# Kernel tuning notes

Hardware: AMD Instinct MI355X
Metric: run time of the kernel (lower is better)

The kernel has to match this reference:

```python
import jax, jax.numpy as jnp
import numpy as np

B, T1, T2, D, H, NL, DFF, NC = 4, 128, 128, 512, 4, 4, 2048, 5
SQRT2 = 1.4142135623730951


def _ln(x, w, b, eps=1e-12):
    m = jnp.mean(x, -1, keepdims=True)
    v = jnp.mean((x - m) ** 2, -1, keepdims=True)
    return w * (x - m) / jnp.sqrt(v + eps) + b


def _gelu(x):  # erf-based gelu, as in source
    return x * 0.5 * (1.0 + jax.lax.erf(x / SQRT2))


def _mha(x, wq, bq, wk, bk, wv, bv, wo, bo):
    b, t, d = x.shape
    dk = d // H
    q = (x @ wq + bq).reshape(b, t, H, dk).transpose(0, 2, 1, 3)
    k = (x @ wk + bk).reshape(b, t, H, dk).transpose(0, 2, 1, 3)
    v = (x @ wv + bv).reshape(b, t, H, dk).transpose(0, 2, 1, 3)
    p = jax.nn.softmax(jnp.einsum('bhqd,bhkd->bhqk', q, k) / jnp.sqrt(jnp.float32(dk)), -1)
    o = jnp.einsum('bhqk,bhkd->bhqd', p, v).transpose(0, 2, 1, 3).reshape(b, t, d)
    return o @ wo + bo


def _encode(x, pos_emb, pe_w, pe_b, Wq, bq, Wk, bk, Wv, bv, Wo, bo,
            ff1_w, ff1_b, ff2_w, ff2_b, lnin_w, lnin_b, lnout_w, lnout_b):
    t = x.shape[1]
    x = _ln(x + pos_emb[:t], pe_w, pe_b)  # PositionalEncoding (dropout=0 eval)
    for i in range(Wq.shape[0]):  # EncoderLayer x NL
        x = x + _mha(x, Wq[i], bq[i], Wk[i], bk[i], Wv[i], bv[i], Wo[i], bo[i])
        h = _ln(x, lnin_w[i], lnin_b[i])
        x = x + (_gelu(h @ ff1_w[i] + ff1_b[i]) @ ff2_w[i] + ff2_b[i])
        x = _ln(x, lnout_w[i], lnout_b[i])
    return x


def _forward(q_emb, a_emb, qa_relation, aq_relation, concept_emb, pos_emb, pe_w, pe_b,
             Wq, bq, Wk, bk, Wv, bv, Wo, bo, ff1_w, ff1_b, ff2_w, ff2_b,
             lnin_w, lnin_b, lnout_w, lnout_b, sim_Wq, sim_bq, sim_Wk, sim_bk, cls_w, cls_b):
    enc = lambda x: _encode(x, pos_emb, pe_w, pe_b, Wq, bq, Wk, bk, Wv, bv, Wo, bo,
                            ff1_w, ff1_b, ff2_w, ff2_b, lnin_w, lnin_b, lnout_w, lnout_b)
    qe = enc(q_emb)   # [B,T1,D]
    ae = enc(a_emb)   # [B,T2,D]
    # ConceptEncoding: relation one-hots -> concept embedding mix
    hL = qa_relation @ concept_emb   # [B,T1,T2,D]
    hR = aq_relation @ concept_emb   # [B,T2,T1,D]
    # SimAttn: note source uses fwK for BOTH key and value, so v == k exactly
    q = qe @ sim_Wq + sim_bq
    k = ae @ sim_Wk + sim_bk
    kR = jnp.transpose(k[:, :, None, :] + hR, (0, 2, 1, 3))  # [B,T1,T2,D]
    scores = jnp.sum((q[:, :, None, :] + hL) * kR, axis=-1)   # [B,T1,T2]
    p = jax.nn.softmax(scores, -1)
    # sharpening branch (default sharpening=True): re-softmax the attention probs
    p = jnp.clip(jax.nn.softmax(1000.0 * p, -1), 0.0, 1.0)
    # value path: v + hR transposed == kR since v == k
    x = jnp.einsum('bts,btsd->btd', p, kR)                    # [B,T1,D]
    return jnp.mean(x, 1) @ cls_w + cls_b                     # [B,3]


def setup_inputs() -> dict:
    key = jax.random.key(0)
    rk = lambda i: jax.random.fold_in(key, i)
    w = lambda i, shape: 0.02 * jax.random.normal(rk(i), shape, jnp.float32)
    z = lambda shape: jnp.zeros(shape, jnp.float32)
    o = lambda shape: jnp.ones(shape, jnp.float32)
    return {
        'q_emb': jax.random.normal(rk(0), (B, T1, D), jnp.float32),
        'a_emb': jax.random.normal(rk(1), (B, T2, D), jnp.float32),
        'qa_relation': jax.random.uniform(rk(2), (B, T1, T2, NC), jnp.float32),
        'aq_relation': jax.random.uniform(rk(3), (B, T2, T1, NC), jnp.float32),
        'concept_emb': w(4, (NC, D)),
        'pos_emb': w(5, (512, D)),
        'pe_w': o((D,)), 'pe_b': z((D,)),
        'Wq': w(6, (NL, D, D)), 'bq': z((NL, D)),
        'Wk': w(7, (NL, D, D)), 'bk': z((NL, D)),
        'Wv': w(8, (NL, D, D)), 'bv': z((NL, D)),
        'Wo': w(9, (NL, D, D)), 'bo': z((NL, D)),
        'ff1_w': w(10, (NL, D, DFF)), 'ff1_b': z((NL, DFF)),
        'ff2_w': w(11, (NL, DFF, D)), 'ff2_b': z((NL, D)),
        'lnin_w': o((NL, D)), 'lnin_b': z((NL, D)),
        'lnout_w': o((NL, D)), 'lnout_b': z((NL, D)),
        'sim_Wq': w(12, (D, D)), 'sim_bq': z((D,)),
        'sim_Wk': w(13, (D, D)), 'sim_bk': z((D,)),
        'cls_w': w(14, (D, 3)), 'cls_b': z((3,)),
    }


def reference(q_emb, a_emb, qa_relation, aq_relation, concept_emb, pos_emb, pe_w, pe_b,
              Wq, bq, Wk, bk, Wv, bv, Wo, bo, ff1_w, ff1_b, ff2_w, ff2_b,
              lnin_w, lnin_b, lnout_w, lnout_b, sim_Wq, sim_bq, sim_Wk, sim_bk, cls_w, cls_b):
    return _forward(q_emb, a_emb, qa_relation, aq_relation, concept_emb, pos_emb, pe_w, pe_b,
                    Wq, bq, Wk, bk, Wv, bv, Wo, bo, ff1_w, ff1_b, ff2_w, ff2_b,
                    lnin_w, lnin_b, lnout_w, lnout_b, sim_Wq, sim_bq, sim_Wk, sim_bk, cls_w, cls_b)
```

## Files before the change

### kernel.cpp

```cpp
#include <hip/hip_runtime.h>
#include <hip/hip_bf16.h>
#include <math.h>

typedef unsigned short u16;
typedef __attribute__((ext_vector_type(8))) short bf16x8;
typedef __attribute__((ext_vector_type(4))) float f32x4;

__device__ __forceinline__ float ldin(const void* p, size_t i, int isbf) {
  if (isbf) return __bfloat162float(((const __hip_bfloat16*)p)[i]);
  return ((const float*)p)[i];
}
__device__ __forceinline__ float bfu(u16 u) { return __builtin_bit_cast(float, (unsigned)u << 16); }
__device__ __forceinline__ u16 f2bf(float x) {
  unsigned u = __builtin_bit_cast(unsigned, x);
  unsigned r = u + 0x7FFFu + ((u >> 16) & 1u);
  return (u16)(r >> 16);
}

__device__ __forceinline__ float wave_sum(float v) {
#pragma unroll
  for (int o = 32; o > 0; o >>= 1) v += __shfl_down(v, o);
  return v;
}

__device__ __forceinline__ float block_sum(float v, float* sbuf) {
  int lane = threadIdx.x & 63;
  int wid = threadIdx.x >> 6;
#pragma unroll
  for (int o = 32; o > 0; o >>= 1) v += __shfl_down(v, o);
  __syncthreads();
  if (lane == 0) sbuf[wid] = v;
  __syncthreads();
  int nw = blockDim.x >> 6;
  if (wid == 0) {
    float r = (lane < nw) ? sbuf[lane] : 0.f;
#pragma unroll
    for (int o = 4; o > 0; o >>= 1) r += __shfl_down(r, o);
    if (lane == 0) sbuf[0] = r;
  }
  __syncthreads();
  return sbuf[0];
}

__device__ __forceinline__ float block_max(float v, float* sbuf) {
  int lane = threadIdx.x & 63;
  int wid = threadIdx.x >> 6;
#pragma unroll
  for (int o = 32; o > 0; o >>= 1) v = fmaxf(v, __shfl_down(v, o));
  __syncthreads();
  if (lane == 0) sbuf[wid] = v;
  __syncthreads();
  int nw = blockDim.x >> 6;
  if (wid == 0) {
    float r = (lane < nw) ? sbuf[lane] : -INFINITY;
#pragma unroll
    for (int o = 4; o > 0; o >>= 1) r = fmaxf(r, __shfl_down(r, o));
    if (lane == 0) sbuf[0] = r;
  }
  __syncthreads();
  return sbuf[0];
}

__global__ void flag_kernel(const void* pe_w, int* flag) {
  if (threadIdx.x == 0 && blockIdx.x == 0)
    *flag = (((const unsigned short*)pe_w)[0] != 0) ? 1 : 0;
}


__global__ __launch_bounds__(256) void convT2(
    const void* __restrict__ S0, const void* __restrict__ S1,
    const void* __restrict__ S2, const void* __restrict__ S3,
    size_t srcStride, int K, int N, u16* __restrict__ Dh, u16* __restrict__ Dl,
    size_t layerStride, size_t tensorStride, int tmask, int lshift,
    const int* __restrict__ dflag) {
  const int isbf = *dflag;
  int z = blockIdx.z;
  int t = z & tmask, l = z >> lshift;
  const void* S = (t == 0) ? S0 : ((t == 1) ? S1 : ((t == 2) ? S2 : S3));
  size_t soff = (size_t)l * srcStride;
  size_t doff = (size_t)l * layerStride + (size_t)t * tensorStride;
  int n0 = blockIdx.x * 32, k0 = blockIdx.y * 32;
  __shared__ float tt[32][33];
  int tx = threadIdx.x & 31, ty = threadIdx.x >> 5;
#pragma unroll
  for (int j = 0; j < 4; ++j) {
    int r = ty + j * 8;
    tt[r][tx] = ldin(S, soff + (size_t)(k0 + r) * N + n0 + tx, isbf);
  }
  __syncthreads();
#pragma unroll
  for (int j = 0; j < 4; ++j) {
    int r = ty + j * 8;
    float v = tt[tx][r];
    u16 h = f2bf(v);
    u16 lo = f2bf(v - bfu(h));
    size_t o = doff + (size_t)(n0 + r) * K + k0 + tx;
    Dh[o] = h;
    Dl[o] = lo;
  }
}

__global__ __launch_bounds__(256) void gemm_hl(
    const u16* __restrict__ Ahp, const u16* __restrict__ Alp, int lda,
    const u16* __restrict__ Whp, const u16* __restrict__ Wlp, int ldw,
    const void* __restrict__ b0, const void* __restrict__ b1, const void* __restrict__ b2,
    size_t bo0, size_t bo1, size_t bo2, int bshift,
    float* __restrict__ C, u16* __restrict__ Chp, u16* __restrict__ Clp,
    u16* __restrict__ Vh, u16* __restrict__ Vl, int ldc,
    int K, int act, int mode, int ysplit, size_t wrowoff1,
    const int* __restrict__ dflag) {
  const int isbf = *dflag;
  __shared__ __align__(16) u16 sAh[64][72];
  __shared__ __align__(16) u16 sAl[64][72];
  __shared__ __align__(16) u16 sBh[64][72];
  __shared__ __align__(16) u16 sBl[64][72];

  int tid = threadIdx.x;
  int by = blockIdx.y;
  int row0 = by * 64, col0 = blockIdx.x * 64;
  int rsplit = (by >= ysplit);
  size_t wrow0 = (size_t)col0 + (rsplit ? wrowoff1 : 0);
  int Ksub = K / (int)gridDim.z;
  int kstart = (int)blockIdx.z * Ksub;
  int addbias = (blockIdx.z == 0);

  int wid = tid >> 6, lane = tid & 63, quad = lane >> 4, lm = lane & 15;
  int mrow = (wid & 1) * 32, ncol = (wid >> 1) * 32;

  f32x4 acc[2][2] = {};

  int sr = tid >> 2, sc = (tid & 3) * 16;

  for (int k0 = kstart; k0 < kstart + Ksub; k0 += 64) {
    const u16* p;
    p = Ahp + (size_t)(row0 + sr) * lda + k0 + sc;
    uint4 a0 = *(const uint4*)p, a1 = *(const uint4*)(p + 8);
    p = Alp + (size_t)(row0 + sr) * lda + k0 + sc;
    uint4 a2 = *(const uint4*)p, a3 = *(const uint4*)(p + 8);
    p = Whp + (wrow0 + sr) * (size_t)ldw + k0 + sc;
    uint4 w0 = *(const uint4*)p, w1 = *(const uint4*)(p + 8);
    p = Wlp + (wrow0 + sr) * (size_t)ldw + k0 + sc;
    uint4 w2 = *(const uint4*)p, w3 = *(const uint4*)(p + 8);
    __syncthreads();
    *(uint4*)&sAh[sr][sc] = a0; *(uint4*)&sAh[sr][sc + 8] = a1;
    *(uint4*)&sAl[sr][sc] = a2; *(uint4*)&sAl[sr][sc + 8] = a3;
    *(uint4*)&sBh[sr][sc] = w0; *(uint4*)&sBh[sr][sc + 8] = w1;
    *(uint4*)&sBl[sr][sc] = w2; *(uint4*)&sBl[sr][sc + 8] = w3;
    __syncthreads();
#pragma unroll
    for (int ks = 0; ks < 2; ++ks) {
      bf16x8 ah[2], al[2], wh[2], wl[2];
#pragma unroll
      for (int mi = 0; mi < 2; ++mi) {
        ah[mi] = *(const bf16x8*)&sAh[mrow + mi * 16 + lm][ks * 32 + quad * 8];
        al[mi] = *(const bf16x8*)&sAl[mrow + mi * 16 + lm][ks * 32 + quad * 8];
      }
#pragma unroll
      for (int ni = 0; ni < 2; ++ni) {
        wh[ni] = *(const bf16x8*)&sBh[ncol + ni * 16 + lm][ks * 32 + quad * 8];
        wl[ni] = *(const bf16x8*)&sBl[ncol + ni * 16 + lm][ks * 32 + quad * 8];
      }
#pragma unroll
      for (int mi = 0; mi < 2; ++mi)
#pragma unroll
        for (int ni = 0; ni < 2; ++ni) {
          acc[mi][ni] = __builtin_amdgcn_mfma_f32_16x16x32_bf16(ah[mi], wh[ni], acc[mi][ni], 0, 0, 0);
          acc[mi][ni] = __builtin_amdgcn_mfma_f32_16x16x32_bf16(al[mi], wh[ni], acc[mi][ni], 0, 0, 0);
          acc[mi][ni] = __builtin_amdgcn_mfma_f32_16x16x32_bf16(ah[mi], wl[ni], acc[mi][ni], 0, 0, 0);
        }
    }
  }
#pragma unroll
  for (int mi = 0; mi < 2; ++mi) {
#pragma unroll
    for (int ni = 0; ni < 2; ++ni) {
      int colg = col0 + ncol + ni * 16 + lm;
      const void* bp; size_t bo;
      if (rsplit) { bp = b1; bo = bo1 + colg; }
      else {
        int seg = colg >> bshift;
        bp = (seg == 0) ? b0 : ((seg == 1) ? b1 : b2);
        bo = (seg == 0) ? bo0 : ((seg == 1) ? bo1 : bo2);
        bo += (size_t)colg - ((size_t)seg << bshift);
      }
      float bv = addbias ? ldin(bp, bo, isbf) : 0.f;
#pragma unroll
      for (int r = 0; r < 4; ++r) {
        int rowg = row0 + mrow + mi * 16 + quad * 4 + r;
        float v = acc[mi][ni][r] + bv;
        if (act) v = v * 0.5f * (1.f + erff(v * 0.70710678118654752f));
        if (mode == 3 && colg >= 1024) {
          int gg = rowg >> 7;
          size_t o = ((size_t)(gg * 512) + (colg - 1024)) * 128 + (rowg & 127);
          u16 hh = f2bf(v); Vh[o] = hh; Vl[o] = f2bf(v - bfu(hh));
        } else {
          size_t o = (size_t)rowg * ldc + colg;
          if (mode == 0) C[o] = v;
          else if (mode == 1) atomicAdd(&C[o], v);
          else if (mode == 4) {
            C[o] = v;
            u16 hh = f2bf(v); Chp[o] = hh; Clp[o] = f2bf(v - bfu(hh));
          } else {
            u16 hh = f2bf(v); Chp[o] = hh; Clp[o] = f2bf(v - bfu(hh));
          }
        }
      }
    }
  }
}

__global__ __launch_bounds__(256) void attn_mfma(
    const u16* __restrict__ Qh, const u16* __restrict__ Ql,
    const u16* __restrict__ Vth, const u16* __restrict__ Vtl,
    u16* __restrict__ Oh, u16* __restrict__ Ol) {
  int tq = blockIdx.x & 3;
  int h = (blockIdx.x >> 2) & 3;
  int g = blockIdx.x >> 4;
  int tid = threadIdx.x;
  int w = tid >> 6, lane = tid & 63, quad = lane >> 4, lm = lane & 15;
  __shared__ float S[32][132];

  f32x4 sacc[2][2] = {};
#pragma unroll
  for (int ks = 0; ks < 4; ++ks) {
    bf16x8 qh[2], ql[2];
#pragma unroll
    for (int mi = 0; mi < 2; ++mi) {
      size_t qi = (size_t)(g * 128 + tq * 32 + mi * 16 + lm) * 1536 + h * 128 + ks * 32 + quad * 8;
      qh[mi] = *(const bf16x8*)(Qh + qi);
      ql[mi] = *(const bf16x8*)(Ql + qi);
    }
#pragma unroll
    for (int ni = 0; ni < 2; ++ni) {
      size_t kix = (size_t)(g * 128 + w * 32 + ni * 16 + lm) * 1536 + 512 + h * 128 + ks * 32 + quad * 8;
      bf16x8 kh = *(const bf16x8*)(Qh + kix);
      bf16x8 kl = *(const bf16x8*)(Ql + kix);
#pragma unroll
      for (int mi = 0; mi < 2; ++mi) {
        sacc[mi][ni] = __builtin_amdgcn_mfma_f32_16x16x32_bf16(qh[mi], kh, sacc[mi][ni], 0, 0, 0);
        sacc[mi][ni] = __builtin_amdgcn_mfma_f32_16x16x32_bf16(ql[mi], kh, sacc[mi][ni], 0, 0, 0);
        sacc[mi][ni] = __builtin_amdgcn_mfma_f32_16x16x32_bf16(qh[mi], kl, sacc[mi][ni], 0, 0, 0);
      }
    }
  }
  const float scale = 0.08838834764831845f;
#pragma unroll
  for (int mi = 0; mi < 2; ++mi)
#pragma unroll
    for (int ni = 0; ni < 2; ++ni)
#pragma unroll
      for (int r = 0; r < 4; ++r)
        S[mi * 16 + quad * 4 + r][w * 32 + ni * 16 + lm] = sacc[mi][ni][r] * scale;
  __syncthreads();

  {
    int row = tid >> 3, j = tid & 7;
    float* sp = &S[row][j * 16];
    float v[16];
    *(float4*)(v) = *(float4*)(sp);
    *(float4*)(v + 4) = *(float4*)(sp + 4);
    *(float4*)(v + 8) = *(float4*)(sp + 8);
    *(float4*)(v + 12) = *(float4*)(sp + 12);
    float mx = v[0];
#pragma unroll
    for (int i = 1; i < 16; ++i) mx = fmaxf(mx, v[i]);
    mx = fmaxf(mx, __shfl_xor(mx, 1));
    mx = fmaxf(mx, __shfl_xor(mx, 2));
    mx = fmaxf(mx, __shfl_xor(mx, 4));
    float sum = 0.f;
#pragma unroll
    for (int i = 0; i < 16; ++i) { v[i] = expf(v[i] - mx); sum += v[i]; }
    sum += __shfl_xor(sum, 1);
    sum += __shfl_xor(sum, 2);
    sum += __shfl_xor(sum, 4);
    float inv = 1.f / sum;
#pragma unroll
    for (int i = 0; i < 16; ++i) v[i] *= inv;
    *(float4*)(sp) = *(float4*)(v);
    *(float4*)(sp + 4) = *(float4*)(v + 4);
    *(float4*)(sp + 8) = *(float4*)(v + 8);
    *(float4*)(sp + 12) = *(float4*)(v + 12);
  }
  __syncthreads();

  f32x4 oacc[2][2] = {};
#pragma unroll
  for (int ks = 0; ks < 4; ++ks) {
    bf16x8 ph[2], pl[2];
#pragma unroll
    for (int mi = 0; mi < 2; ++mi) {
      float pv[8];
      const float* srow = &S[mi * 16 + lm][ks * 32 + quad * 8];
      *(float4*)(pv) = *(const float4*)srow;
      *(float4*)(pv + 4) = *(const float4*)(srow + 4);
      bf16x8 hh, ll;
#pragma unroll
      for (int i = 0; i < 8; ++i) {
        u16 hb = f2bf(pv[i]);
        hh[i] = (short)hb;
        ll[i] = (short)f2bf(pv[i] - bfu(hb));
      }
      ph[mi] = hh; pl[mi] = ll;
    }
#pragma unroll
    for (int ni = 0; ni < 2; ++ni) {
      size_t vi = (size_t)(g * 512 + h * 128 + w * 32 + ni * 16 + lm) * 128 + ks * 32 + quad * 8;
      bf16x8 vh = *(const bf16x8*)(Vth + vi);
      bf16x8 vl = *(const bf16x8*)(Vtl + vi);
#pragma unroll
      for (int mi = 0; mi < 2; ++mi) {
        oacc[mi][ni] = __builtin_amdgcn_mfma_f32_16x16x32_bf16(ph[mi], vh, oacc[mi][ni], 0, 0, 0);
        oacc[mi][ni] = __builtin_amdgcn_mfma_f32_16x16x32_bf16(pl[mi], vh, oacc[mi][ni], 0, 0, 0);
        oacc[mi][ni] = __builtin_amdgcn_mfma_f32_16x16x32_bf16(ph[mi], vl, oacc[mi][ni], 0, 0, 0);
      }
    }
  }
#pragma unroll
  for (int mi = 0; mi < 2; ++mi)
#pragma unroll
    for (int ni = 0; ni < 2; ++ni)
#pragma unroll
      for (int r = 0; r < 4; ++r) {
        int t = tq * 32 + mi * 16 + quad * 4 + r;
        int d = w * 32 + ni * 16 + lm;
        size_t o = (size_t)(g * 128 + t) * 512 + h * 128 + d;
        float val = oacc[mi][ni][r];
        u16 hb = f2bf(val);
        Oh[o] = hb;
        Ol[o] = f2bf(val - bfu(hb));
      }
}

__global__ __launch_bounds__(256) void emb_ln2(
    const void* __restrict__ qe, const void* __restrict__ ae, const void* __restrict__ pos,
    const void* __restrict__ w, const void* __restrict__ b,
    float* __restrict__ x, u16* __restrict__ oh, u16* __restrict__ ol,
    const int* __restrict__ dflag) {
  const int isbf = *dflag;
  const int D = 512;
  int row = blockIdx.x;
  const void* emb = (row < 512) ? qe : ae;
  int lr = row & 511, t = row & 127;
  __shared__ float sbuf[8];
  int i0 = threadIdx.x, i1 = threadIdx.x + 256;
  float v0 = ldin(emb, (size_t)lr * D + i0, isbf) + ldin(pos, (size_t)t * D + i0, isbf);
  float v1 = ldin(emb, (size_t)lr * D + i1, isbf) + ldin(pos, (size_t)t * D + i1, isbf);
  float mean = block_sum(v0 + v1, sbuf) / 512.f;
  float d0 = v0 - mean, d1 = v1 - mean;
  float var = block_sum(d0 * d0 + d1 * d1, sbuf) / 512.f;
  float inv = 1.0f / sqrtf(var + 1e-12f);
  float r0 = ldin(w, i0, isbf) * d0 * inv + ldin(b, i0, isbf);
  float r1 = ldin(w, i1, isbf) * d1 * inv + ldin(b, i1, isbf);
  size_t o0 = (size_t)row * D + i0, o1 = (size_t)row * D + i1;
  x[o0] = r0; x[o1] = r1;
  u16 h0 = f2bf(r0); oh[o0] = h0; ol[o0] = f2bf(r0 - bfu(h0));
  u16 h1 = f2bf(r1); oh[o1] = h1; ol[o1] = f2bf(r1 - bfu(h1));
}

__global__ __launch_bounds__(256) void ln2(
    const float* __restrict__ in, float* __restrict__ outf,
    u16* __restrict__ oh, u16* __restrict__ ol,
    const void* __restrict__ w, const void* __restrict__ b, size_t wboff,
    const int* __restrict__ dflag) {
  const int isbf = *dflag;
  const int D = 512;
  int row = blockIdx.x;
  __shared__ float sbuf[8];
  int i0 = threadIdx.x, i1 = threadIdx.x + 256;
  float v0 = in[(size_t)row * D + i0];
  float v1 = in[(size_t)row * D + i1];
  float mean = block_sum(v0 + v1, sbuf) / 512.f;
  float d0 = v0 - mean, d1 = v1 - mean;
  float var = block_sum(d0 * d0 + d1 * d1, sbuf) / 512.f;
  float inv = 1.0f / sqrtf(var + 1e-12f);
  float r0 = ldin(w, wboff + i0, isbf) * d0 * inv + ldin(b, wboff + i0, isbf);
  float r1 = ldin(w, wboff + i1, isbf) * d1 * inv + ldin(b, wboff + i1, isbf);
  size_t o0 = (size_t)row * D + i0, o1 = (size_t)row * D + i1;
  if (outf) { outf[o0] = r0; outf[o1] = r1; }
  u16 h0 = f2bf(r0); oh[o0] = h0; ol[o0] = f2bf(r0 - bfu(h0));
  u16 h1 = f2bf(r1); oh[o1] = h1; ol[o1] = f2bf(r1 - bfu(h1));
}

__global__ __launch_bounds__(64) void projgram(const float* __restrict__ qkb,
                                               const void* __restrict__ ce,
                                               float* __restrict__ ck, float* __restrict__ G,
                                               const int* __restrict__ dflag) {
  const int isbf = *dflag;
  if (blockIdx.x < 1024) {
    int row = blockIdx.x;
#pragma unroll
    for (int c = 0; c < 5; ++c) {
      float acc = 0.f;
      for (int d = threadIdx.x; d < 512; d += 64)
        acc = fmaf(qkb[(size_t)row * 512 + d], ldin(ce, (size_t)c * 512 + d, isbf), acc);
      acc = wave_sum(acc);
      if (threadIdx.x == 0) ck[row * 5 + c] = acc;
    }
  } else {
    int i = blockIdx.x - 1024;
    int c = i / 5, c2 = i % 5;
    float acc = 0.f;
    for (int d = threadIdx.x; d < 512; d += 64)
      acc = fmaf(ldin(ce, (size_t)c * 512 + d, isbf), ldin(ce, (size_t)c2 * 512 + d, isbf), acc);
    acc = wave_sum(acc);
    if (threadIdx.x == 0) G[i] = acc;
  }
}

__global__ __launch_bounds__(256) void prep_rel(
    const void* __restrict__ aq, const float* __restrict__ ck, const float* __restrict__ G,
    float* __restrict__ mT, float* __restrict__ nT, const int* __restrict__ dflag) {
  const int isbf = *dflag;
  int bx = blockIdx.x;
  int t0 = (bx & 3) * 32;
  int s0 = ((bx >> 2) & 3) * 32;
  int b = bx >> 4;
  int tid = threadIdx.x;
  __shared__ float aqs[32][164];
  __shared__ float Gs[25];
  __shared__ float kcs[32][5];
  __shared__ float qcs[32][5];
  for (int i = tid; i < 5120; i += 256) {
    int s = i / 160, r = i % 160;
    aqs[s][r] = ldin(aq, ((size_t)(b * 128 + s0 + s) * 128 + t0) * 5 + r, isbf);
  }
  if (tid < 25) Gs[tid] = G[tid];
  for (int i = tid; i < 160; i += 256)
    kcs[i / 5][i % 5] = ck[(size_t)(512 + b * 128 + s0 + i / 5) * 5 + i % 5];
  for (int i = tid; i < 160; i += 256)
    qcs[i / 5][i % 5] = ck[(size_t)(b * 128 + t0 + i / 5) * 5 + i % 5];
  __syncthreads();
  for (int i = tid; i < 5120; i += 256) {
    int t = i / 160, j = i % 160, s = j / 5, c = j % 5;
    float ga = 0.f;
#pragma unroll
    for (int c2 = 0; c2 < 5; ++c2) ga = fmaf(Gs[c * 5 + c2], aqs[s][t * 5 + c2], ga);
    mT[((size_t)(b * 128 + t0 + t) * 128 + s0 + s) * 5 + c] = kcs[s][c] + ga;
  }
  for (int i = tid; i < 1024; i += 256) {
    int t = i >> 5, s = i & 31;
    float n = 0.f;
#pragma unroll
    for (int c = 0; c < 5; ++c) n = fmaf(aqs[s][t * 5 + c], qcs[t][c], n);
    nT[(size_t)(b * 128 + t0 + t) * 128 + s0 + s] = n;
  }
}

__global__ __launch_bounds__(256) void scores_mfma(
    const u16* __restrict__ Qh, const u16* __restrict__ Ql,
    const void* __restrict__ qa, const float* __restrict__ mT, const float* __restrict__ nT,
    float* __restrict__ P, const int* __restrict__ dflag) {
  const int isbf = *dflag;
  int tq = blockIdx.x & 3;
  int b = blockIdx.x >> 2;
  int tid = threadIdx.x;
  int w = tid >> 6, lane = tid & 63, quad = lane >> 4, lm = lane & 15;
  __shared__ float S[32][132];

  f32x4 sacc[2][2] = {};
#pragma unroll
  for (int ks = 0; ks < 16; ++ks) {
    bf16x8 qh[2], ql[2];
#pragma unroll
    for (int mi = 0; mi < 2; ++mi) {
      size_t qi = (size_t)(b * 128 + tq * 32 + mi * 16 + lm) * 512 + ks * 32 + quad * 8;
      qh[mi] = *(const bf16x8*)(Qh + qi);
      ql[mi] = *(const bf16x8*)(Ql + qi);
    }
#pragma unroll
    for (int ni = 0; ni < 2; ++ni) {
      size_t ki = (size_t)(512 + b * 128 + w * 32 + ni * 16 + lm) * 512 + ks * 32 + quad * 8;
      bf16x8 kh = *(const bf16x8*)(Qh + ki);
      bf16x8 kl = *(const bf16x8*)(Ql + ki);
#pragma unroll
      for (int mi = 0; mi < 2; ++mi) {
        sacc[mi][ni] = __builtin_amdgcn_mfma_f32_16x16x32_bf16(qh[mi], kh, sacc[mi][ni], 0, 0, 0);
        sacc[mi][ni] = __builtin_amdgcn_mfma_f32_16x16x32_bf16(ql[mi], kh, sacc[mi][ni], 0, 0, 0);
        sacc[mi][ni] = __builtin_amdgcn_mfma_f32_16x16x32_bf16(qh[mi], kl, sacc[mi][ni], 0, 0, 0);
      }
    }
  }
#pragma unroll
  for (int mi = 0; mi < 2; ++mi)
#pragma unroll
    for (int ni = 0; ni < 2; ++ni)
#pragma unroll
      for (int r = 0; r < 4; ++r)
        S[mi * 16 + quad * 4 + r][w * 32 + ni * 16 + lm] = sacc[mi][ni][r];
  __syncthreads();

  {
    int t = tid >> 3;
    int s0 = (tid & 7) * 16;
    size_t gt = (size_t)(b * 128 + tq * 32 + t);
    for (int s = s0; s < s0 + 16; ++s) {
      size_t o = gt * 128 + s;
      float r = nT[o];
      size_t o5 = o * 5;
#pragma unroll
      for (int c = 0; c < 5; ++c) r = fmaf(ldin(qa, o5 + c, isbf), mT[o5 + c], r);
      S[t][s] += r;
    }
  }
  __syncthreads();

  {
    int row = tid >> 3, j = tid & 7;
    float* sp = &S[row][j * 16];
    float v[16];
    *(float4*)(v) = *(float4*)(sp);
    *(float4*)(v + 4) = *(float4*)(sp + 4);
    *(float4*)(v + 8) = *(float4*)(sp + 8);
    *(float4*)(v + 12) = *(float4*)(sp + 12);
    float mx = v[0];
#pragma unroll
    for (int i = 1; i < 16; ++i) mx = fmaxf(mx, v[i]);
    mx = fmaxf(mx, __shfl_xor(mx, 1));
    mx = fmaxf(mx, __shfl_xor(mx, 2));
    mx = fmaxf(mx, __shfl_xor(mx, 4));
    float sum = 0.f;
#pragma unroll
    for (int i = 0; i < 16; ++i) { v[i] = expf(v[i] - mx); sum += v[i]; }
    sum += __shfl_xor(sum, 1);
    sum += __shfl_xor(sum, 2);
    sum += __shfl_xor(sum, 4);
    float inv = 1.f / sum;
#pragma unroll
    for (int i = 0; i < 16; ++i) v[i] *= inv;
    float mx2 = v[0];
#pragma unroll
    for (int i = 1; i < 16; ++i) mx2 = fmaxf(mx2, v[i]);
    mx2 = fmaxf(mx2, __shfl_xor(mx2, 1));
    mx2 = fmaxf(mx2, __shfl_xor(mx2, 2));
    mx2 = fmaxf(mx2, __shfl_xor(mx2, 4));
    float sum2 = 0.f;
#pragma unroll
    for (int i = 0; i < 16; ++i) { v[i] = expf(1000.f * (v[i] - mx2)); sum2 += v[i]; }
    sum2 += __shfl_xor(sum2, 1);
    sum2 += __shfl_xor(sum2, 2);
    sum2 += __shfl_xor(sum2, 4);
    float inv2 = 1.f / sum2;
#pragma unroll
    for (int i = 0; i < 16; ++i) v[i] = fminf(fmaxf(v[i] * inv2, 0.f), 1.f);
    float* pp = P + ((size_t)(b * 128 + tq * 32 + row)) * 128 + j * 16;
    *(float4*)(pp) = *(float4*)(v);
    *(float4*)(pp + 4) = *(float4*)(v + 4);
    *(float4*)(pp + 8) = *(float4*)(v + 8);
    *(float4*)(pp + 12) = *(float4*)(v + 12);
  }
}

__global__ __launch_bounds__(512) void meancls(
    const float* __restrict__ qkb, const float* __restrict__ P, const void* __restrict__ aq,
    const void* __restrict__ ce, const void* __restrict__ clsw, const void* __restrict__ clsb,
    void* __restrict__ out, const int* __restrict__ dflag) {
  const int isbf = *dflag;
  int b = blockIdx.x;
  int tid = threadIdx.x;
  __shared__ float Ps[128];
  __shared__ float pas[5];
  __shared__ float xm[512];
  __shared__ float sbuf[8];
  if (tid < 5) pas[tid] = 0.f;
  __syncthreads();
  {
    int s = tid >> 2, jj = tid & 3;
    float pac[5] = {0.f, 0.f, 0.f, 0.f, 0.f};
    for (int t = jj * 32; t < jj * 32 + 32; ++t) {
      float pv = P[((size_t)(b * 128 + t)) * 128 + s];
      size_t ao = ((size_t)(b * 128 + s) * 128 + t) * 5;
#pragma unroll
      for (int c = 0; c < 5; ++c) pac[c] = fmaf(pv, ldin(aq, ao + c, isbf), pac[c]);
    }
#pragma unroll
    for (int c = 0; c < 5; ++c) {
      float v = wave_sum(pac[c]);
      if ((tid & 63) == 0) atomicAdd(&pas[c], v);
    }
  }
  if (tid < 128) {
    float a = 0.f;
    for (int t = 0; t < 128; ++t) a += P[((size_t)(b * 128 + t)) * 128 + tid];
    Ps[tid] = a;
  }
  __syncthreads();
  int d = tid;
  const float* k = qkb + (size_t)(512 + b * 128) * 512 + d;
  float acc = 0.f;
  for (int s = 0; s < 128; ++s) acc = fmaf(Ps[s], k[(size_t)s * 512], acc);
#pragma unroll
  for (int c = 0; c < 5; ++c) acc = fmaf(pas[c], ldin(ce, (size_t)c * 512 + d, isbf), acc);
  acc *= (1.f / 128.f);
  xm[d] = acc;
  __syncthreads();
  for (int j = 0; j < 3; ++j) {
    float v = block_sum(xm[d] * ldin(clsw, (size_t)d * 3 + j, isbf), sbuf);
    if (d == 0) {
      float val = v + ldin(clsb, j, isbf);
      if (isbf) ((u16*)out)[b * 3 + j] = f2bf(val);
      else ((float*)out)[b * 3 + j] = val;
    }
    __syncthreads();
  }
}


__global__ __launch_bounds__(256) void gemm_mfma(
    const float* __restrict__ A, const void* __restrict__ W, size_t woff,
    const void* __restrict__ bias, size_t boff,
    float* __restrict__ C, int M, int N, int K, int act, int addto,
    const int* __restrict__ dflag) {
  const int isbf = *dflag;
  __shared__ __align__(16) u16 Ah[64][40];
  __shared__ __align__(16) u16 Al[64][40];
  __shared__ __align__(16) u16 Wh[64][40];
  __shared__ __align__(16) u16 Wl[64][40];
  int tid = threadIdx.x;
  int row0 = blockIdx.y * 64, col0 = blockIdx.x * 64;
  int wid = tid >> 6, lane = tid & 63;
  int quad = lane >> 4, lm = lane & 15;
  int mrow = (wid & 1) * 32, ncol = (wid >> 1) * 32;
  f32x4 acc[2][2] = {};
  int ar = tid >> 2, akc = (tid & 3) * 8;
  int bk = tid >> 3, bn0 = (tid & 7) * 8;
  for (int k0 = 0; k0 < K; k0 += 32) {
    const float* ap = A + (size_t)(row0 + ar) * K + k0 + akc;
    float av[8];
    *(float4*)(av) = *(const float4*)ap;
    *(float4*)(av + 4) = *(const float4*)(ap + 4);
    unsigned hp[4], lp[4];
#pragma unroll
    for (int j = 0; j < 4; ++j) {
      u16 h0 = f2bf(av[2 * j]);
      u16 h1 = f2bf(av[2 * j + 1]);
      u16 l0 = f2bf(av[2 * j] - bfu(h0));
      u16 l1 = f2bf(av[2 * j + 1] - bfu(h1));
      hp[j] = (unsigned)h0 | ((unsigned)h1 << 16);
      lp[j] = (unsigned)l0 | ((unsigned)l1 << 16);
    }
    *(uint4*)&Ah[ar][akc] = make_uint4(hp[0], hp[1], hp[2], hp[3]);
    *(uint4*)&Al[ar][akc] = make_uint4(lp[0], lp[1], lp[2], lp[3]);
    float wv[8];
    size_t welem = woff + (size_t)(k0 + bk) * N + col0 + bn0;
    if (isbf) {
      const u16* wp = (const u16*)W + welem;
      uint4 raw = *(const uint4*)wp;
      wv[0] = bfu((u16)(raw.x & 0xFFFF)); wv[1] = bfu((u16)(raw.x >> 16));
      wv[2] = bfu((u16)(raw.y & 0xFFFF)); wv[3] = bfu((u16)(raw.y >> 16));
      wv[4] = bfu((u16)(raw.z & 0xFFFF)); wv[5] = bfu((u16)(raw.z >> 16));
      wv[6] = bfu((u16)(raw.w & 0xFFFF)); wv[7] = bfu((u16)(raw.w >> 16));
    } else {
      const float* wp = (const float*)W + welem;
      *(float4*)(wv) = *(const float4*)wp;
      *(float4*)(wv + 4) = *(const float4*)(wp + 4);
    }
#pragma unroll
    for (int i = 0; i < 8; ++i) {
      u16 h = f2bf(wv[i]);
      u16 l = f2bf(wv[i] - bfu(h));
      Wh[bn0 + i][bk] = h;
      Wl[bn0 + i][bk] = l;
    }
    __syncthreads();
#pragma unroll
    for (int mi = 0; mi < 2; ++mi) {
      bf16x8 ah = *(const bf16x8*)&Ah[mrow + mi * 16 + lm][quad * 8];
      bf16x8 al = *(const bf16x8*)&Al[mrow + mi * 16 + lm][quad * 8];
#pragma unroll
      for (int ni = 0; ni < 2; ++ni) {
        bf16x8 wh = *(const bf16x8*)&Wh[ncol + ni * 16 + lm][quad * 8];
        bf16x8 wl = *(const bf16x8*)&Wl[ncol + ni * 16 + lm][quad * 8];
        acc[mi][ni] = __builtin_amdgcn_mfma_f32_16x16x32_bf16(ah, wh, acc[mi][ni], 0, 0, 0);
        acc[mi][ni] = __builtin_amdgcn_mfma_f32_16x16x32_bf16(al, wh, acc[mi][ni], 0, 0, 0);
        acc[mi][ni] = __builtin_amdgcn_mfma_f32_16x16x32_bf16(ah, wl, acc[mi][ni], 0, 0, 0);
      }
    }
    __syncthreads();
  }
#pragma unroll
  for (int mi = 0; mi < 2; ++mi) {
#pragma unroll
    for (int ni = 0; ni < 2; ++ni) {
      int colg = col0 + ncol + ni * 16 + lm;
      float bv = ldin(bias, boff + colg, isbf);
#pragma unroll
      for (int r = 0; r < 4; ++r) {
        int rowg = row0 + mrow + mi * 16 + quad * 4 + r;
        float v = acc[mi][ni][r] + bv;
        if (act) v = v * 0.5f * (1.f + erff(v * 0.70710678118654752f));
        size_t o = (size_t)rowg * N + colg;
        if (addto) C[o] += v; else C[o] = v;
      }
    }
  }
}

__global__ __launch_bounds__(256) void emb_ln_kernel(const void* __restrict__ emb,
                                                     const void* __restrict__ pos,
                                                     const void* __restrict__ w,
                                                     const void* __restrict__ b,
                                                     float* __restrict__ out, int T, int D,
                                                     const int* __restrict__ dflag) {
  const int isbf = *dflag;
  int row = blockIdx.x;
  int t = row % T;
  __shared__ float sbuf[8];
  int i0 = threadIdx.x, i1 = threadIdx.x + 256;
  float v0 = ldin(emb, (size_t)row * D + i0, isbf) + ldin(pos, (size_t)t * D + i0, isbf);
  float v1 = ldin(emb, (size_t)row * D + i1, isbf) + ldin(pos, (size_t)t * D + i1, isbf);
  float mean = block_sum(v0 + v1, sbuf) / (float)D;
  float d0 = v0 - mean, d1 = v1 - mean;
  float var = block_sum(d0 * d0 + d1 * d1, sbuf) / (float)D;
  float inv = 1.0f / sqrtf(var + 1e-12f);
  out[(size_t)row * D + i0] = ldin(w, i0, isbf) * d0 * inv + ldin(b, i0, isbf);
  out[(size_t)row * D + i1] = ldin(w, i1, isbf) * d1 * inv + ldin(b, i1, isbf);
}

__global__ __launch_bounds__(256) void ln_kernel(const float* __restrict__ in, float* __restrict__ out,
                                                 const void* __restrict__ w, const void* __restrict__ b,
                                                 size_t wboff, int D, const int* __restrict__ dflag) {
  const int isbf = *dflag;
  int row = blockIdx.x;
  __shared__ float sbuf[8];
  int i0 = threadIdx.x, i1 = threadIdx.x + 256;
  float v0 = in[(size_t)row * D + i0];
  float v1 = in[(size_t)row * D + i1];
  float mean = block_sum(v0 + v1, sbuf) / (float)D;
  float d0 = v0 - mean, d1 = v1 - mean;
  float var = block_sum(d0 * d0 + d1 * d1, sbuf) / (float)D;
  float inv = 1.0f / sqrtf(var + 1e-12f);
  out[(size_t)row * D + i0] = ldin(w, wboff + i0, isbf) * d0 * inv + ldin(b, wboff + i0, isbf);
  out[(size_t)row * D + i1] = ldin(w, wboff + i1, isbf) * d1 * inv + ldin(b, wboff + i1, isbf);
}

__global__ __launch_bounds__(128) void attn_kernel(const float* __restrict__ q, const float* __restrict__ k,
                                                   const float* __restrict__ v, float* __restrict__ o,
                                                   int B, int H, int T, int dk) {
  int t = blockIdx.x % T;
  int h = (blockIdx.x / T) % H;
  int b = blockIdx.x / (T * H);
  int D = H * dk;
  int tid = threadIdx.x;
  __shared__ float qs[128];
  __shared__ float ps[128];
  __shared__ float sbuf[8];
  qs[tid] = q[(size_t)(b * T + t) * D + h * dk + tid];
  __syncthreads();
  const float* krow = k + (size_t)(b * T + tid) * D + h * dk;
  float sc = 0.f;
#pragma unroll 8
  for (int d = 0; d < 128; ++d) sc = fmaf(qs[d], krow[d], sc);
  sc *= 0.08838834764831845f;
  float mx = block_max(sc, sbuf);
  float e = expf(sc - mx);
  float s = block_sum(e, sbuf);
  ps[tid] = e / s;
  __syncthreads();
  float acc = 0.f;
  for (int s2 = 0; s2 < 128; ++s2)
    acc = fmaf(ps[s2], v[(size_t)(b * T + s2) * D + h * dk + tid], acc);
  o[(size_t)(b * T + t) * D + h * dk + tid] = acc;
}

__global__ __launch_bounds__(64) void proj_ce_kernel(const float* __restrict__ q,
                                                     const void* __restrict__ ce,
                                                     float* __restrict__ out, int D, int NC,
                                                     const int* __restrict__ dflag) {
  const int isbf = *dflag;
  int row = blockIdx.x;
  for (int c = 0; c < NC; ++c) {
    float acc = 0.f;
    for (int d = threadIdx.x; d < D; d += 64)
      acc = fmaf(q[(size_t)row * D + d], ldin(ce, (size_t)c * D + d, isbf), acc);
    acc = wave_sum(acc);
    if (threadIdx.x == 0) out[row * NC + c] = acc;
  }
}

__global__ __launch_bounds__(64) void gram_kernel(const void* __restrict__ ce,
                                                  float* __restrict__ G, int D, int NC,
                                                  const int* __restrict__ dflag) {
  const int isbf = *dflag;
  int c = blockIdx.x / NC, c2 = blockIdx.x % NC;
  float acc = 0.f;
  for (int d = threadIdx.x; d < D; d += 64)
    acc = fmaf(ldin(ce, (size_t)c * D + d, isbf), ldin(ce, (size_t)c2 * D + d, isbf), acc);
  acc = wave_sum(acc);
  if (threadIdx.x == 0) G[blockIdx.x] = acc;
}

__global__ __launch_bounds__(128) void sim_scores_kernel(
    const float* __restrict__ q, const float* __restrict__ k, const void* __restrict__ qa,
    const void* __restrict__ aq, const float* __restrict__ qc, const float* __restrict__ kc,
    const float* __restrict__ G, float* __restrict__ p_out, float* __restrict__ pa_out,
    int B, int T1, int T2, int D, int NC, const int* __restrict__ dflag) {
  const int isbf = *dflag;
  int t = blockIdx.x % T1;
  int b = blockIdx.x / T1;
  int s = threadIdx.x;
  __shared__ float qs[512];
  __shared__ float Gs[25];
  __shared__ float qcs[5];
  __shared__ float sbuf[8];
  for (int i = threadIdx.x; i < D; i += 128) qs[i] = q[(size_t)(b * T1 + t) * D + i];
  if (threadIdx.x < NC * NC) Gs[threadIdx.x] = G[threadIdx.x];
  if (threadIdx.x < NC) qcs[threadIdx.x] = qc[(b * T1 + t) * NC + threadIdx.x];
  __syncthreads();
  const float* krow = k + (size_t)(b * T2 + s) * D;
  float sc = 0.f;
#pragma unroll 8
  for (int d = 0; d < 512; ++d) sc = fmaf(qs[d], krow[d], sc);
  float qav[5], aqv[5];
#pragma unroll
  for (int c = 0; c < 5; ++c) {
    qav[c] = ldin(qa, (size_t)((b * T1 + t) * T2 + s) * NC + c, isbf);
    aqv[c] = ldin(aq, (size_t)((b * T2 + s) * T1 + t) * NC + c, isbf);
  }
#pragma unroll
  for (int c = 0; c < 5; ++c) {
    sc = fmaf(aqv[c], qcs[c], sc);
    sc = fmaf(qav[c], kc[(b * T2 + s) * NC + c], sc);
#pragma unroll
    for (int c2 = 0; c2 < 5; ++c2) sc = fmaf(qav[c] * Gs[c * 5 + c2], aqv[c2], sc);
  }
  float mx = block_max(sc, sbuf);
  float e = expf(sc - mx);
  float ssum = block_sum(e, sbuf);
  float p = e / ssum;
  float mx2 = block_max(p, sbuf);
  float e2 = expf(1000.f * (p - mx2));
  float s2 = block_sum(e2, sbuf);
  float pf = fminf(fmaxf(e2 / s2, 0.f), 1.f);
  p_out[(size_t)(b * T1 + t) * T2 + s] = pf;
#pragma unroll
  for (int c = 0; c < 5; ++c) {
    float pc = block_sum(pf * aqv[c], sbuf);
    if (threadIdx.x == 0) pa_out[(b * T1 + t) * NC + c] = pc;
  }
}

__global__ __launch_bounds__(512) void sim_x_kernel(const float* __restrict__ p, const float* __restrict__ k,
                                                    const float* __restrict__ pa,
                                                    const void* __restrict__ ce,
                                                    float* __restrict__ x, int B, int T1, int T2, int D, int NC,
                                                    const int* __restrict__ dflag) {
  const int isbf = *dflag;
  int t = blockIdx.x % T1;
  int b = blockIdx.x / T1;
  int d = threadIdx.x;
  __shared__ float ps[128];
  __shared__ float pav[5];
  if (threadIdx.x < T2) ps[threadIdx.x] = p[(size_t)(b * T1 + t) * T2 + threadIdx.x];
  if (threadIdx.x < NC) pav[threadIdx.x] = pa[(b * T1 + t) * NC + threadIdx.x];
  __syncthreads();
  float acc = 0.f;
  for (int s = 0; s < 128; ++s) acc = fmaf(ps[s], k[(size_t)(b * T2 + s) * D + d], acc);
#pragma unroll
  for (int c = 0; c < 5; ++c) acc = fmaf(pav[c], ldin(ce, (size_t)c * D + d, isbf), acc);
  x[(size_t)(b * T1 + t) * D + d] = acc;
}

__global__ __launch_bounds__(512) void mean_kernel(const float* __restrict__ x, float* __restrict__ xm,
                                                   int T, int D) {
  int b = blockIdx.x;
  int d = threadIdx.x;
  float acc = 0.f;
  for (int t = 0; t < T; ++t) acc += x[(size_t)(b * T + t) * D + d];
  xm[(size_t)b * D + d] = acc / (float)T;
}

__global__ __launch_bounds__(64) void cls_kernel(const float* __restrict__ xm,
                                                 const void* __restrict__ w,
                                                 const void* __restrict__ bias,
                                                 void* __restrict__ out, int D, int NO,
                                                 const int* __restrict__ dflag) {
  const int isbf = *dflag;
  int j = blockIdx.x % NO;
  int b = blockIdx.x / NO;
  float acc = 0.f;
  for (int d = threadIdx.x; d < D; d += 64)
    acc = fmaf(xm[(size_t)b * D + d], ldin(w, (size_t)d * NO + j, isbf), acc);
  acc = wave_sum(acc);
  if (threadIdx.x == 0) {
    float val = acc + ldin(bias, j, isbf);
    if (isbf) ((__hip_bfloat16*)out)[b * NO + j] = __float2bfloat16(val);
    else ((float*)out)[b * NO + j] = val;
  }
}

extern "C" void kernel_launch(void* const* d_in, const int* in_sizes, int n_in,
                              void* d_out, int out_size, void* d_ws, size_t ws_size,
                              hipStream_t stream) {
  const int B = 4, T = 128, D = 512, H = 4, NL = 4, DFF = 2048, NC = 5;
  const void *q_emb = d_in[0], *a_emb = d_in[1], *qa = d_in[2], *aqr = d_in[3],
             *ce = d_in[4], *pos = d_in[5], *pe_w = d_in[6], *pe_b = d_in[7],
             *Wq = d_in[8], *bq = d_in[9], *Wk = d_in[10], *bk = d_in[11],
             *Wv = d_in[12], *bv = d_in[13], *Wo = d_in[14], *bo = d_in[15],
             *ff1w = d_in[16], *ff1b = d_in[17], *ff2w = d_in[18], *ff2b = d_in[19],
             *lnin_w = d_in[20], *lnin_b = d_in[21], *lnout_w = d_in[22], *lnout_b = d_in[23],
             *simWq = d_in[24], *simbq = d_in[25], *simWk = d_in[26], *simbk = d_in[27],
             *clsw = d_in[28], *clsb = d_in[29];

  const size_t REQ = 82000000ull;
  if (ws_size >= REQ) {
    char* base = (char*)d_ws;
    float* x = (float*)(base + 0);
    u16* xch = (u16*)(base + 2097152);
    u16* xcl = (u16*)(base + 3145728);
    u16* qkvh = (u16*)(base + 4194304);
    u16* qkvl = (u16*)(base + 7340032);
    u16* ffch = (u16*)(base + 10485760);
    u16* ffcl = (u16*)(base + 14680064);
    u16* Vth = (u16*)(base + 18874368);
    u16* Vtl = (u16*)(base + 19922944);
    float* qkb = (float*)(base + 20971520);
    u16* qsh = (u16*)(base + 23068672);
    u16* qsl = (u16*)(base + 24117248);
    float* ck = (float*)(base + 25165824);
    float* Gbuf = (float*)(base + 25186304);
    int* dflag = (int*)(base + 25196544);
    u16* wh = (u16*)(base + 26214400);
    u16* wl = (u16*)(base + 52428800);
    float* P = (float*)(base + 79691776);
    float* mT = (float*)(base + 79953920);
    float* nT = (float*)(base + 81264640);

    flag_kernel<<<1, 64, 0, stream>>>(pe_w, dflag);
    convT2<<<dim3(16, 16, 16), 256, 0, stream>>>(Wq, Wk, Wv, Wo, 262144, 512, 512,
                                                 wh, wl, 3145728, 262144, 3, 2, dflag);
    convT2<<<dim3(64, 16, 4), 256, 0, stream>>>(ff1w, ff1w, ff1w, ff1w, 1048576, 512, 2048,
                                                wh + 1048576, wl + 1048576, 3145728, 0, 0, 0, dflag);
    convT2<<<dim3(16, 64, 4), 256, 0, stream>>>(ff2w, ff2w, ff2w, ff2w, 1048576, 2048, 512,
                                                wh + 2097152, wl + 2097152, 3145728, 0, 0, 0, dflag);
    convT2<<<dim3(16, 16, 2), 256, 0, stream>>>(simWq, simWk, simWk, simWk, 0, 512, 512,
                                                wh + 12582912, wl + 12582912, 0, 262144, 1, 1, dflag);

    emb_ln2<<<1024, 256, 0, stream>>>(q_emb, a_emb, pos, pe_w, pe_b, x, xch, xcl, dflag);

    for (int l = 0; l < NL; ++l) {
      size_t wbase = (size_t)l * 3145728, bD = (size_t)l * D;
      gemm_hl<<<dim3(24, 16, 1), 256, 0, stream>>>(xch, xcl, 512, wh + wbase, wl + wbase, 512,
                                                   bq, bk, bv, bD, bD, bD, 9,
                                                   nullptr, qkvh, qkvl, Vth, Vtl, 1536,
                                                   512, 0, 3, 9999, 0, dflag);
      attn_mfma<<<128, 256, 0, stream>>>(qkvh, qkvl, Vth, Vtl, xch, xcl);
      gemm_hl<<<dim3(8, 16, 2), 256, 0, stream>>>(xch, xcl, 512, wh + wbase + 786432,
                                                  wl + wbase + 786432, 512,
                                                  bo, bo, bo, bD, bD, bD, 9,
                                                  x, nullptr, nullptr, nullptr, nullptr, 512,
                                                  512, 0, 1, 9999, 0, dflag);
      ln2<<<1024, 256, 0, stream>>>(x, nullptr, xch, xcl, lnin_w, lnin_b, bD, dflag);
      gemm_hl<<<dim3(32, 16, 1), 256, 0, stream>>>(xch, xcl, 512, wh + wbase + 1048576,
                                                   wl + wbase + 1048576, 512,
                                                   ff1b, ff1b, ff1b,
                                                   (size_t)l * DFF, (size_t)l * DFF, (size_t)l * DFF, 11,
                                                   nullptr, ffch, ffcl, nullptr, nullptr, 2048,
                                                   512, 1, 2, 9999, 0, dflag);
      gemm_hl<<<dim3(8, 16, 2), 256, 0, stream>>>(ffch, ffcl, 2048, wh + wbase + 2097152,
                                                  wl + wbase + 2097152, 2048,
                                                  ff2b, ff2b, ff2b, bD, bD, bD, 9,
                                                  x, nullptr, nullptr, nullptr, nullptr, 512,
                                                  2048, 0, 1, 9999, 0, dflag);
      ln2<<<1024, 256, 0, stream>>>(x, x, xch, xcl, lnout_w, lnout_b, bD, dflag);
    }

    gemm_hl<<<dim3(8, 16, 1), 256, 0, stream>>>(xch, xcl, 512, wh + 12582912, wl + 12582912, 512,
                                                simbq, simbk, simbk, 0, 0, 0, 9,
                                                qkb, qsh, qsl, nullptr, nullptr, 512,
                                                512, 0, 4, 8, 512, dflag);
    projgram<<<1049, 64, 0, stream>>>(qkb, ce, ck, Gbuf, dflag);
    prep_rel<<<64, 256, 0, stream>>>(aqr, ck, Gbuf, mT, nT, dflag);
    scores_mfma<<<16, 256, 0, stream>>>(qsh, qsl, qa, mT, nT, P, dflag);
    meancls<<<4, 512, 0, stream>>>(qkb, P, aqr, ce, clsw, clsb, d_out, dflag);
    return;
  }

  float* ws = (float*)d_ws;
  const size_t S = (size_t)512 * 512;
  float* qe = ws;
  float* ae = ws + S;
  float* hb = ws + 2 * S;
  float* rb = ws + 3 * S;
  float* qb = rb;
  float* kb = rb + S;
  float* vb = rb + 2 * S;
  float* ob = rb + 3 * S;
  float* ffb = rb;
  float* pbuf = rb + 2 * S;
  float* pabuf = pbuf + 65536;
  float* qcbuf = pabuf + 2560;
  float* kcbuf = qcbuf + 2560;
  float* Gbuf = kcbuf + 2560;
  float* xmean = Gbuf + 32;
  float* xsim = rb + 3 * S;
  int* dflag = (int*)(ws + 7 * S);

  const int M = B * T;
  dim3 gD(8, 8), gF1(32, 8), gF2(8, 8);

  flag_kernel<<<1, 64, 0, stream>>>(pe_w, dflag);
  for (int e = 0; e < 2; ++e) {
    float* x = (e == 0) ? qe : ae;
    const void* emb = (e == 0) ? q_emb : a_emb;
    emb_ln_kernel<<<M, 256, 0, stream>>>(emb, pos, pe_w, pe_b, x, T, D, dflag);
    for (int l = 0; l < NL; ++l) {
      size_t wDD = (size_t)l * D * D, bD = (size_t)l * D;
      gemm_mfma<<<gD, 256, 0, stream>>>(x, Wq, wDD, bq, bD, qb, M, D, D, 0, 0, dflag);
      gemm_mfma<<<gD, 256, 0, stream>>>(x, Wk, wDD, bk, bD, kb, M, D, D, 0, 0, dflag);
      gemm_mfma<<<gD, 256, 0, stream>>>(x, Wv, wDD, bv, bD, vb, M, D, D, 0, 0, dflag);
      attn_kernel<<<B * H * T, 128, 0, stream>>>(qb, kb, vb, ob, B, H, T, D / H);
      gemm_mfma<<<gD, 256, 0, stream>>>(ob, Wo, wDD, bo, bD, x, M, D, D, 0, 1, dflag);
      ln_kernel<<<M, 256, 0, stream>>>(x, hb, lnin_w, lnin_b, bD, D, dflag);
      gemm_mfma<<<gF1, 256, 0, stream>>>(hb, ff1w, (size_t)l * D * DFF, ff1b, (size_t)l * DFF,
                                         ffb, M, DFF, D, 1, 0, dflag);
      gemm_mfma<<<gF2, 256, 0, stream>>>(ffb, ff2w, (size_t)l * DFF * D, ff2b, bD,
                                         x, M, D, DFF, 0, 1, dflag);
      ln_kernel<<<M, 256, 0, stream>>>(x, x, lnout_w, lnout_b, bD, D, dflag);
    }
  }
  gemm_mfma<<<gD, 256, 0, stream>>>(qe, simWq, 0, simbq, 0, qb, M, D, D, 0, 0, dflag);
  gemm_mfma<<<gD, 256, 0, stream>>>(ae, simWk, 0, simbk, 0, kb, M, D, D, 0, 0, dflag);
  proj_ce_kernel<<<M, 64, 0, stream>>>(qb, ce, qcbuf, D, NC, dflag);
  proj_ce_kernel<<<M, 64, 0, stream>>>(kb, ce, kcbuf, D, NC, dflag);
  gram_kernel<<<NC * NC, 64, 0, stream>>>(ce, Gbuf, D, NC, dflag);
  sim_scores_kernel<<<B * T, 128, 0, stream>>>(qb, kb, qa, aqr, qcbuf, kcbuf, Gbuf, pbuf, pabuf,
                                               B, T, T, D, NC, dflag);
  sim_x_kernel<<<B * T, 512, 0, stream>>>(pbuf, kb, pabuf, ce, xsim, B, T, T, D, NC, dflag);
  mean_kernel<<<B, 512, 0, stream>>>(xsim, xmean, T, D);
  cls_kernel<<<B * 3, 64, 0, stream>>>(xmean, clsw, clsb, d_out, D, 3, dflag);
}
```

Before: 664.0 us.

## Fuse P column sums and relation-weighted reductions into scores kernel

The scores kernel now computes, in-block, the column sums of the probability matrix and the aq-relation-weighted per-concept sums, then accumulates them atomically into small global buffers. meancls reads these instead of re-reading the full P matrix and doing strided loads over aq. prep_rel additionally writes a transposed copy of aq so the fused reduction can read it contiguously, and a combined init kernel zeroes the accumulators. This removes the full P round trip and meancls's serial reductions, at the cost of an extra aqT write, more work in the 16-block scores kernel, and float atomics that make summation order nondeterministic.

```diff
diff --git a/kernel.cpp b/kernel.cpp
--- a/kernel.cpp
+++ b/kernel.cpp
@@ -64,6 +64,13 @@
 __global__ void flag_kernel(const void* pe_w, int* flag) {
   if (threadIdx.x == 0 && blockIdx.x == 0)
     *flag = (((const unsigned short*)pe_w)[0] != 0) ? 1 : 0;
+}
+
+__global__ void init_kernel(const void* pe_w, int* flag, float* Pbar, float* pabar) {
+  int t = threadIdx.x;
+  if (t == 0) *flag = (((const unsigned short*)pe_w)[0] != 0) ? 1 : 0;
+  if (t < 512) Pbar[t] = 0.f;
+  if (t < 20) pabar[t] = 0.f;
 }
 
 
@@ -409,7 +416,8 @@
 
 __global__ __launch_bounds__(256) void prep_rel(
     const void* __restrict__ aq, const float* __restrict__ ck, const float* __restrict__ G,
-    float* __restrict__ mT, float* __restrict__ nT, const int* __restrict__ dflag) {
+    float* __restrict__ mT, float* __restrict__ nT, float* __restrict__ aqT,
+    const int* __restrict__ dflag) {
   const int isbf = *dflag;
   int bx = blockIdx.x;
   int t0 = (bx & 3) * 32;
@@ -432,10 +440,13 @@
   __syncthreads();
   for (int i = tid; i < 5120; i += 256) {
     int t = i / 160, j = i % 160, s = j / 5, c = j % 5;
+    float av = aqs[s][t * 5 + c];
     float ga = 0.f;
 #pragma unroll
     for (int c2 = 0; c2 < 5; ++c2) ga = fmaf(Gs[c * 5 + c2], aqs[s][t * 5 + c2], ga);
-    mT[((size_t)(b * 128 + t0 + t) * 128 + s0 + s) * 5 + c] = kcs[s][c] + ga;
+    size_t o = ((size_t)(b * 128 + t0 + t) * 128 + s0 + s) * 5 + c;
+    mT[o] = kcs[s][c] + ga;
+    aqT[o] = av;
   }
   for (int i = tid; i < 1024; i += 256) {
     int t = i >> 5, s = i & 31;
@@ -449,13 +460,16 @@
 __global__ __launch_bounds__(256) void scores_mfma(
     const u16* __restrict__ Qh, const u16* __restrict__ Ql,
     const void* __restrict__ qa, const float* __restrict__ mT, const float* __restrict__ nT,
-    float* __restrict__ P, const int* __restrict__ dflag) {
+    const float* __restrict__ aqT, float* __restrict__ Pbar, float* __restrict__ pabar,
+    const int* __restrict__ dflag) {
   const int isbf = *dflag;
   int tq = blockIdx.x & 3;
   int b = blockIdx.x >> 2;
   int tid = threadIdx.x;
   int w = tid >> 6, lane = tid & 63, quad = lane >> 4, lm = lane & 15;
   __shared__ float S[32][132];
+  __shared__ float pas[5];
+  if (tid < 5) pas[tid] = 0.f;
 
   f32x4 sacc[2][2] = {};
 #pragma unroll
@@ -542,16 +556,36 @@
     float inv2 = 1.f / sum2;
 #pragma unroll
     for (int i = 0; i < 16; ++i) v[i] = fminf(fmaxf(v[i] * inv2, 0.f), 1.f);
-    float* pp = P + ((size_t)(b * 128 + tq * 32 + row)) * 128 + j * 16;
-    *(float4*)(pp) = *(float4*)(v);
-    *(float4*)(pp + 4) = *(float4*)(v + 4);
-    *(float4*)(pp + 8) = *(float4*)(v + 8);
-    *(float4*)(pp + 12) = *(float4*)(v + 12);
-  }
+    *(float4*)(sp) = *(float4*)(v);
+    *(float4*)(sp + 4) = *(float4*)(v + 4);
+    *(float4*)(sp + 8) = *(float4*)(v + 8);
+    *(float4*)(sp + 12) = *(float4*)(v + 12);
+    float pac[5] = {0.f, 0.f, 0.f, 0.f, 0.f};
+    const float* aqt = aqT + ((size_t)(b * 128 + tq * 32 + row) * 128 + j * 16) * 5;
+#pragma unroll
+    for (int i = 0; i < 16; ++i) {
+      float pv = v[i];
+#pragma unroll
+      for (int c = 0; c < 5; ++c) pac[c] = fmaf(pv, aqt[i * 5 + c], pac[c]);
+    }
+#pragma unroll
+    for (int c = 0; c < 5; ++c) {
+      float pv = wave_sum(pac[c]);
+      if (lane == 0) atomicAdd(&pas[c], pv);
+    }
+  }
+  __syncthreads();
+  if (tid < 128) {
+    float cs = 0.f;
+#pragma unroll 8
+    for (int t = 0; t < 32; ++t) cs += S[t][tid];
+    atomicAdd(&Pbar[b * 128 + tid], cs);
+  }
+  if (tid < 5) atomicAdd(&pabar[b * 5 + tid], pas[tid]);
 }
 
 __global__ __launch_bounds__(512) void meancls(
-    const float* __restrict__ qkb, const float* __restrict__ P, const void* __restrict__ aq,
+    const float* __restrict__ qkb, const float* __restrict__ Pbar, const float* __restrict__ pabar,
     const void* __restrict__ ce, const void* __restrict__ clsw, const void* __restrict__ clsb,
     void* __restrict__ out, const int* __restrict__ dflag) {
   const int isbf = *dflag;
@@ -561,28 +595,8 @@
   __shared__ float pas[5];
   __shared__ float xm[512];
   __shared__ float sbuf[8];
-  if (tid < 5) pas[tid] = 0.f;
-  __syncthreads();
-  {
-    int s = tid >> 2, jj = tid & 3;
-    float pac[5] = {0.f, 0.f, 0.f, 0.f, 0.f};
-    for (int t = jj * 32; t < jj * 32 + 32; ++t) {
-      float pv = P[((size_t)(b * 128 + t)) * 128 + s];
-      size_t ao = ((size_t)(b * 128 + s) * 128 + t) * 5;
-#pragma unroll
-      for (int c = 0; c < 5; ++c) pac[c] = fmaf(pv, ldin(aq, ao + c, isbf), pac[c]);
-    }
-#pragma unroll
-    for (int c = 0; c < 5; ++c) {
-      float v = wave_sum(pac[c]);
-      if ((tid & 63) == 0) atomicAdd(&pas[c], v);
-    }
-  }
-  if (tid < 128) {
-    float a = 0.f;
-    for (int t = 0; t < 128; ++t) a += P[((size_t)(b * 128 + t)) * 128 + tid];
-    Ps[tid] = a;
-  }
+  if (tid < 128) Ps[tid] = Pbar[b * 128 + tid];
+  if (tid < 5) pas[tid] = pabar[b * 5 + tid];
   __syncthreads();
   int d = tid;
   const float* k = qkb + (size_t)(512 + b * 128) * 512 + d;
@@ -901,7 +915,7 @@
              *simWq = d_in[24], *simbq = d_in[25], *simWk = d_in[26], *simbk = d_in[27],
              *clsw = d_in[28], *clsb = d_in[29];
 
-  const size_t REQ = 82000000ull;
+  const size_t REQ = 83000000ull;
   if (ws_size >= REQ) {
     char* base = (char*)d_ws;
     float* x = (float*)(base + 0);
@@ -918,14 +932,16 @@
     u16* qsl = (u16*)(base + 24117248);
     float* ck = (float*)(base + 25165824);
     float* Gbuf = (float*)(base + 25186304);
+    float* Pbar = (float*)(base + 25190400);
+    float* pabar = (float*)(base + 25192448);
     int* dflag = (int*)(base + 25196544);
     u16* wh = (u16*)(base + 26214400);
     u16* wl = (u16*)(base + 52428800);
-    float* P = (float*)(base + 79691776);
-    float* mT = (float*)(base + 79953920);
-    float* nT = (float*)(base + 81264640);
-
-    flag_kernel<<<1, 64, 0, stream>>>(pe_w, dflag);
+    float* aqT = (float*)(base + 79691776);
+    float* mT = (float*)(base + 81002496);
+    float* nT = (float*)(base + 82313216);
+
+    init_kernel<<<1, 512, 0, stream>>>(pe_w, dflag, Pbar, pabar);
     convT2<<<dim3(16, 16, 16), 256, 0, stream>>>(Wq, Wk, Wv, Wo, 262144, 512, 512,
                                                  wh, wl, 3145728, 262144, 3, 2, dflag);
     convT2<<<dim3(64, 16, 4), 256, 0, stream>>>(ff1w, ff1w, ff1w, ff1w, 1048576, 512, 2048,
@@ -969,9 +985,9 @@
                                                 qkb, qsh, qsl, nullptr, nullptr, 512,
                                                 512, 0, 4, 8, 512, dflag);
     projgram<<<1049, 64, 0, stream>>>(qkb, ce, ck, Gbuf, dflag);
-    prep_rel<<<64, 256, 0, stream>>>(aqr, ck, Gbuf, mT, nT, dflag);
-    scores_mfma<<<16, 256, 0, stream>>>(qsh, qsl, qa, mT, nT, P, dflag);
-    meancls<<<4, 512, 0, stream>>>(qkb, P, aqr, ce, clsw, clsb, d_out, dflag);
+    prep_rel<<<64, 256, 0, stream>>>(aqr, ck, Gbuf, mT, nT, aqT, dflag);
+    scores_mfma<<<16, 256, 0, stream>>>(qsh, qsl, qa, mT, nT, aqT, Pbar, pabar, dflag);
+    meancls<<<4, 512, 0, stream>>>(qkb, Pbar, pabar, ce, clsw, clsb, d_out, dflag);
     return;
   }
 
```

New measurement: 626.9 us. -5.6%, faster.
